# Kernel optimization log

Hardware: AMD Instinct MI355X
Metric: run time of the kernel (lower is better)

## Reference

```python
import jax, jax.numpy as jnp
import numpy as np
from jax import lax

EPS = 1e-5

def _conv(x, w, b, pad):
    # NCHW conv, stride 1, symmetric padding `pad`
    y = lax.conv_general_dilated(x, w, window_strides=(1, 1),
                                 padding=[(pad, pad), (pad, pad)],
                                 dimension_numbers=('NCHW', 'OIHW', 'NCHW'))
    return y + b[None, :, None, None]

def _bn(x, gamma, beta):
    # BatchNorm2d, training mode: batch statistics over (N,H,W)
    mean = jnp.mean(x, axis=(0, 2, 3), keepdims=True)
    var = jnp.var(x, axis=(0, 2, 3), keepdims=True)
    return gamma[None, :, None, None] * (x - mean) * lax.rsqrt(var + EPS) + beta[None, :, None, None]

def setup_inputs() -> dict:
    key = jax.random.key(0)
    ks = jax.random.split(key, 8)
    B, C, H, W = 4, 256, 64, 64
    OC = 256
    s3 = 1.0 / np.sqrt(C * 9)
    s1 = 1.0 / np.sqrt(C)
    return {
        'x': jax.random.normal(ks[0], (B, C, H, W), jnp.float32),
        'Wq': jax.random.normal(ks[1], (OC, C, 3, 3), jnp.float32) * s3,
        'bq': jnp.zeros((OC,), jnp.float32),
        'gq': jnp.ones((OC,), jnp.float32),
        'betaq': jnp.zeros((OC,), jnp.float32),
        'Wk': jax.random.normal(ks[2], (OC, C, 1, 1), jnp.float32) * s1,
        'bk': jnp.zeros((OC,), jnp.float32),
        'gk': jnp.ones((OC,), jnp.float32),
        'betak': jnp.zeros((OC,), jnp.float32),
        'Wv': jax.random.normal(ks[3], (OC, C, 1, 1), jnp.float32) * s1,
        'bv': jnp.zeros((OC,), jnp.float32),
        'gv': jnp.ones((OC,), jnp.float32),
        'betav': jnp.zeros((OC,), jnp.float32),
    }

def reference(x, Wq, bq, gq, betaq, Wk, bk, gk, betak, Wv, bv, gv, betav):
    # Q: 3x3 conv, pad 1 -> (b, oc, h, w); K,V: 1x1 conv with pad 1 -> (b, oc, h+2, w+2)
    Q = _bn(_conv(x, Wq, bq, 1), gq, betaq)
    K = _bn(_conv(x, Wk, bk, 1), gk, betak)
    V = _bn(_conv(x, Wv, bv, 1), gv, betav)
    b, oc, oh, ow = Q.shape
    q = Q.reshape(b, oc, oh * ow)          # (b, c, q_tokens)
    k = K.reshape(b, oc, -1)               # (b, c, k_tokens)
    v = V.reshape(b, oc, -1)               # (b, c, k_tokens)
    scores = jnp.einsum('bck,bcq->bkq', k, q)      # (b, k_tokens, q_tokens)
    attn = jax.nn.softmax(scores, axis=1)          # softmax over key tokens (dim=1)
    out = jnp.einsum('bck,bkq->bcq', v, attn)      # (b, c, q_tokens)
    return out.reshape(b, oc, oh, ow)
```

## Files before the change

kernel.cpp:

```cpp
#include <hip/hip_runtime.h>


typedef unsigned short u16;
typedef _Float16 f16x8 __attribute__((ext_vector_type(8)));
typedef __attribute__((ext_vector_type(4))) float f32x4;

__device__ __forceinline__ u16 f2h(float f) {
  _Float16 h = (_Float16)f;
  return *(const u16*)&h;
}
__device__ __forceinline__ float bf2f(u16 h) {
  return __uint_as_float(((unsigned)h) << 16);
}
__device__ __forceinline__ float ldin(const void* p, size_t i, int f32) {
  return f32 ? ((const float*)p)[i] : bf2f(((const u16*)p)[i]);
}
__device__ __forceinline__ u16 f2bf(float f) {
  unsigned u = __float_as_uint(f);
  u += 0x7fffu + ((u >> 16) & 1u);
  return (u16)(u >> 16);
}
__device__ __forceinline__ void gld16(const void* g, void* l) {
  __builtin_amdgcn_global_load_lds(
      (const __attribute__((address_space(1))) unsigned int*)g,
      (__attribute__((address_space(3))) unsigned int*)l, 16, 0, 0);
}

__global__ __launch_bounds__(256) void k_detect(const unsigned* __restrict__ w,
                                                int* __restrict__ flag) {
  __shared__ int red[4];
  int tid = threadIdx.x, cnt = 0;
#pragma unroll
  for (int j = 0; j < 8; j++) {
    unsigned e = (w[tid + j * 8192] >> 7) & 0xFFu;
    cnt += (e >= 118u && e <= 127u) ? 1 : 0;
  }
#pragma unroll
  for (int off = 32; off; off >>= 1) cnt += __shfl_down(cnt, off);
  if ((tid & 63) == 0) red[tid >> 6] = cnt;
  __syncthreads();
  if (tid == 0)
    flag[0] = (red[0] + red[1] + red[2] + red[3] < 625) ? 1 : 0;
}

__global__ __launch_bounds__(256) void k_txp(const void* __restrict__ x,
                                             const int* __restrict__ flag,
                                             u16* __restrict__ xbTp) {
  __shared__ float tile[32][33];
  int f32 = flag[0];
  int b = blockIdx.z, p0 = blockIdx.x * 32, c0 = blockIdx.y * 32;
  int tx = threadIdx.x, ty = threadIdx.y;
#pragma unroll
  for (int i = 0; i < 4; i++) {
    int c = c0 + ty + i * 8, pp = p0 + tx;
    float v = 0.f;
    if (pp < 4356) {
      int yy = pp / 66, xx = pp - yy * 66;
      if (yy >= 1 && yy <= 64 && xx >= 1 && xx <= 64)
        v = ldin(x, ((size_t)b * 256 + c) * 4096 + (yy - 1) * 64 + (xx - 1), f32);
    }
    tile[ty + i * 8][tx] = v;
  }
  __syncthreads();
#pragma unroll
  for (int i = 0; i < 4; i++) {
    int pp = p0 + ty + i * 8;
    if (pp >= 4356) continue;
    xbTp[((size_t)b * 4356 + pp) * 256 + c0 + tx] = f2h(tile[tx][ty + i * 8]);
  }
}

__global__ __launch_bounds__(256) void k_wq(const void* __restrict__ Wq,
                                            const int* __restrict__ flag,
                                            u16* __restrict__ WqB) {
  int idx = blockIdx.x * 256 + threadIdx.x;
  int oc = idx / 2304, rem = idx - oc * 2304;
  int tap = rem >> 8, c = rem & 255;
  WqB[idx] = f2h(ldin(Wq, oc * 2304 + c * 9 + tap, flag[0]));
}
__global__ __launch_bounds__(256) void k_wkv(const void* __restrict__ Wk,
                                             const void* __restrict__ Wv,
                                             const int* __restrict__ flag,
                                             u16* __restrict__ WkvB) {
  int idx = blockIdx.x * 256 + threadIdx.x;
  int m = idx >> 8, c = idx & 255;
  float w = (m < 256) ? ldin(Wk, m * 256 + c, flag[0])
                      : ldin(Wv, (m - 256) * 256 + c, flag[0]);
  WkvB[idx] = f2h(w);
}

template <bool IMC, int EPI, int SWZ>
__global__ __launch_bounds__(256, 3) void gemm_bt(
    const u16* __restrict__ A, const u16* __restrict__ Bt, void* __restrict__ Cptr,
    int M, int N, int K, int ldB, int tapBase, long long cOff, int kChunk,
    int sw1, int sw2, int nSplit, long long zA, long long zB, long long zC) {
  __shared__ u16 lA[128 * 64];
  __shared__ u16 lB[128 * 64];
  int tm, tn, b = 0, kz = 0;
  if (SWZ == 1) {
    int lin = blockIdx.x, xcd = lin & 7, per = lin >> 3;
    tm = xcd * sw1 + (per % sw1);
    tn = per / sw1;
    b = blockIdx.y;
  } else if (SWZ == 2) {
    int lin = blockIdx.x, xcd = lin & 7, per = lin >> 3;
    tm = per % sw1;
    tn = xcd * sw2 + per / sw1;
    kz = blockIdx.z;
  } else {
    tm = blockIdx.x;
    tn = blockIdx.y;
    b = blockIdx.z / nSplit;
    kz = blockIdx.z % nSplit;
  }
  int k0 = 0, k1 = K;
  if (kChunk) {
    k0 = kz * kChunk;
    k1 = min(k0 + kChunk, K);
  }
  const int tid = threadIdx.x, wave = tid >> 6, lane = tid & 63;
  const int sr = lane >> 3;
  const int scw = (lane & 7) ^ sr;
  const int wm = (wave >> 1) * 64, wn = (wave & 1) * 64;
  const int r16 = lane & 15, q = lane >> 4;
  const u16* gA = A + (size_t)b * zA + (size_t)(tm * 128 + wave * 32 + sr) * K +
                  scw * 8;
  const u16* gB = nullptr;
  int pyI[4], pxI[4];
  size_t bOffI[4];
  if (IMC) {
#pragma unroll
    for (int i = 0; i < 4; i++) {
      int n = tn * 128 + wave * 32 + i * 8 + sr;
      int bb = n >> 12, pix = n & 4095;
      pyI[i] = pix >> 6;
      pxI[i] = pix & 63;
      bOffI[i] = (size_t)bb * 4356;
    }
  } else {
    gB = Bt + (size_t)b * zB + (size_t)(tn * 128 + wave * 32 + sr) * ldB +
         scw * 8;
  }
  f32x4 acc[4][4] = {};

  for (int kt = k0; kt < k1; kt += 64) {
    int dy = 0, dx = 0, chunk = 0;
    if (IMC) {
      int tap = tapBase + (kt >> 8);
      chunk = kt & 255;
      dy = tap / 3;
      dx = tap - dy * 3;
    }
#pragma unroll
    for (int i = 0; i < 4; i++) {
      gld16(gA + (size_t)(i * 8) * K + kt, &lA[(wave * 32 + i * 8) * 64]);
      if (IMC) {
        int spix = (pyI[i] + dy) * 66 + pxI[i] + dx;
        gld16(Bt + (bOffI[i] + spix) * 256 + chunk + scw * 8,
              &lB[(wave * 32 + i * 8) * 64]);
      } else {
        gld16(gB + (size_t)(i * 8) * ldB + kt, &lB[(wave * 32 + i * 8) * 64]);
      }
    }
    __syncthreads();
#pragma unroll
    for (int ks = 0; ks < 64; ks += 32) {
      f16x8 af[4], bfr[4];
#pragma unroll
      for (int f = 0; f < 4; f++) {
        int ma = wm + f * 16 + r16;
        int g = (ks >> 3) + q;
        af[f] = *(const f16x8*)&lA[ma * 64 + ((g ^ (ma & 7)) << 3)];
        int nb = wn + f * 16 + r16;
        bfr[f] = *(const f16x8*)&lB[nb * 64 + ((g ^ (nb & 7)) << 3)];
      }
#pragma unroll
      for (int fi = 0; fi < 4; fi++)
#pragma unroll
        for (int fj = 0; fj < 4; fj++)
          acc[fi][fj] = __builtin_amdgcn_mfma_f32_16x16x32_f16(
              af[fi], bfr[fj], acc[fi][fj], 0, 0, 0);
    }
    __syncthreads();
  }

  const int colB = tn * 128 + wn + r16;
  const int rowB = tm * 128 + wm + q * 4;
  float* C = (float*)Cptr + cOff + (size_t)b * zC;
  if (EPI == 0) {
#pragma unroll
    for (int fi = 0; fi < 4; fi++)
#pragma unroll
      for (int r = 0; r < 4; r++) {
        size_t ro = (size_t)(rowB + fi * 16 + r) * N;
#pragma unroll
        for (int fj = 0; fj < 4; fj++) C[ro + colB + fj * 16] = acc[fi][fj][r];
      }
  } else {
#pragma unroll
    for (int fi = 0; fi < 4; fi++)
#pragma unroll
      for (int r = 0; r < 4; r++) {
        size_t ro = (size_t)(rowB + fi * 16 + r) * N;
#pragma unroll
        for (int fj = 0; fj < 4; fj++)
          atomicAdd(&C[ro + colB + fj * 16], acc[fi][fj][r]);
      }
  }
}

__global__ __launch_bounds__(256) void k_stats(
    const float* __restrict__ bufQ, const float* __restrict__ bufKV,
    const void* __restrict__ gq, const void* __restrict__ betaq,
    const void* __restrict__ gk, const void* __restrict__ betak,
    const void* __restrict__ gv, const void* __restrict__ betav,
    const int* __restrict__ flag, float* __restrict__ nrm) {
  int f32 = flag[0];
  int ch = blockIdx.x, t = blockIdx.y, tid = threadIdx.x;
  const float* row = (t == 0) ? bufQ + (size_t)ch * 16384
                              : bufKV + (size_t)(t == 1 ? ch : 256 + ch) * 16384;
  float s = 0.f, ss = 0.f;
  for (int i = tid; i < 16384; i += 256) {
    float v = row[i];
    s += v;
    ss += v * v;
  }
#pragma unroll
  for (int off = 32; off; off >>= 1) {
    s += __shfl_down(s, off);
    ss += __shfl_down(ss, off);
  }
  __shared__ float ls[4], lss[4];
  if ((tid & 63) == 0) {
    ls[tid >> 6] = s;
    lss[tid >> 6] = ss;
  }
  __syncthreads();
  if (tid == 0) {
    s = ls[0] + ls[1] + ls[2] + ls[3];
    ss = lss[0] + lss[1] + lss[2] + lss[3];
    float cnt = (t == 0) ? 16384.f : 17424.f;
    float mean = s / cnt;
    float var = fmaxf(ss / cnt - mean * mean, 0.f);
    const void* g = (t == 0) ? gq : (t == 1 ? gk : gv);
    const void* be = (t == 0) ? betaq : (t == 1 ? betak : betav);
    float sc = ldin(g, ch, f32) * rsqrtf(var + 1e-5f);
    nrm[(t * 256 + ch) * 2] = sc;
    nrm[(t * 256 + ch) * 2 + 1] = ldin(be, ch, f32) - mean * sc;
  }
}

__global__ __launch_bounds__(256) void k_qTs(const float* __restrict__ bufQ,
                                             const float* __restrict__ nrm,
                                             u16* __restrict__ qTs) {
  __shared__ u16 th[32][33];
  int b = blockIdx.z, q0 = blockIdx.x * 32, c0 = blockIdx.y * 32;
  int tx = threadIdx.x, ty = threadIdx.y;
#pragma unroll
  for (int i = 0; i < 4; i++) {
    int c = c0 + ty + i * 8;
    float sc = nrm[c * 2], sh = nrm[c * 2 + 1];
    th[ty + i * 8][tx] =
        f2h(bufQ[(size_t)c * 16384 + b * 4096 + q0 + tx] * sc + sh);
  }
  __syncthreads();
#pragma unroll
  for (int i = 0; i < 4; i++)
    qTs[((size_t)b * 4096 + q0 + ty + i * 8) * 256 + c0 + tx] =
        th[tx][ty + i * 8];
}
__global__ __launch_bounds__(256) void k_kTs(const float* __restrict__ bufKV,
                                             const float* __restrict__ nrm,
                                             u16* __restrict__ kTs) {
  __shared__ u16 th[32][33];
  int b = blockIdx.z, k0 = blockIdx.x * 32, c0 = blockIdx.y * 32;
  int tx = threadIdx.x, ty = threadIdx.y;
#pragma unroll
  for (int i = 0; i < 4; i++) {
    int c = c0 + ty + i * 8;
    int kt = k0 + tx;
    float v = 0.f;
    if (kt < 4356) {
      float sc = nrm[(256 + c) * 2], sh = nrm[(256 + c) * 2 + 1];
      int yy = kt / 66, xx = kt - yy * 66;
      if (yy >= 1 && yy <= 64 && xx >= 1 && xx <= 64)
        v = bufKV[(size_t)c * 16384 + b * 4096 + (yy - 1) * 64 + (xx - 1)] * sc + sh;
      else
        v = sh;
    }
    th[ty + i * 8][tx] = f2h(v);
  }
  __syncthreads();
#pragma unroll
  for (int i = 0; i < 4; i++)
    kTs[((size_t)b * 4480 + k0 + ty + i * 8) * 256 + c0 + tx] =
        th[tx][ty + i * 8];
}

__global__ __launch_bounds__(256) void k_vP(const float* __restrict__ bufKV,
                                            const float* __restrict__ nrm,
                                            u16* __restrict__ vP) {
  int b = blockIdx.z, ch = blockIdx.y;
  int kt = blockIdx.x * 256 + threadIdx.x;
  if (kt >= 4480) return;
  float v = 0.f;
  if (kt < 4356) {
    float sc = nrm[(512 + ch) * 2], sh = nrm[(512 + ch) * 2 + 1];
    int yy = kt / 66, xx = kt - yy * 66;
    if (yy >= 1 && yy <= 64 && xx >= 1 && xx <= 64)
      v = bufKV[(size_t)(256 + ch) * 16384 + b * 4096 + (yy - 1) * 64 + (xx - 1)] * sc + sh;
    else
      v = sh;
  }
  vP[((size_t)b * 256 + ch) * 4480 + kt] = f2h(v);
}

__global__ __launch_bounds__(256, 2) void k_flash(
    const u16* __restrict__ qTs, const u16* __restrict__ kTs,
    const u16* __restrict__ vP, float* __restrict__ Op,
    float* __restrict__ ml) {
  __shared__ u16 lS[2][16384];
  __shared__ u16 lP[64 * 128];
  const int lin = blockIdx.x;
  const int xcd = lin & 7, per = lin >> 3;
  const int h = xcd & 1, b = xcd >> 1;
  const int qt0 = per * 64;
  const int tid = threadIdx.x, wave = tid >> 6, lane = tid & 63;
  const int sr = lane >> 3, scw = (lane & 7) ^ sr;
  const int r16 = lane & 15, q = lane >> 4;

  const u16* gQ = qTs + ((size_t)b * 4096 + qt0 + wave * 16 + r16) * 256;
  f16x8 aq[8];
#pragma unroll
  for (int kk = 0; kk < 8; kk++) aq[kk] = *(const f16x8*)&gQ[kk * 32 + q * 8];
  asm volatile("s_waitcnt vmcnt(0)" ::: "memory");

  const u16* gK = kTs + (size_t)b * 4480 * 256 + (size_t)(wave * 32 + sr) * 256 + scw * 8;
  const u16* gV = vP + ((size_t)b * 256 + wave * 64 + sr) * 4480 + scw * 8;

#define STAGE_K(buf, kt, c2)                                                 \
  {                                                                          \
    _Pragma("unroll") for (int i = 0; i < 4; i++) {                          \
      const u16* src = gK + (size_t)((kt) + i * 8) * 256 + (c2) * 128;       \
      gld16(src, &lS[buf][(wave * 32 + i * 8) * 64]);                        \
      gld16(src + 64, &lS[buf][8192 + (wave * 32 + i * 8) * 64]);            \
    }                                                                        \
  }
#define STAGE_V(buf, kt, vc)                                                 \
  {                                                                          \
    _Pragma("unroll") for (int i = 0; i < 8; i++)                            \
        gld16(gV + (size_t)(i * 8) * 4480 + (kt) + (vc) * 64,                \
              &lS[buf][(wave * 64 + i * 8) * 64]);                           \
  }
#define WAITB(n)                                                             \
  asm volatile("s_waitcnt vmcnt(" #n ")" ::: "memory");                      \
  __builtin_amdgcn_s_barrier();                                              \
  __builtin_amdgcn_sched_barrier(0);
#define CLOSEB()                                                             \
  __builtin_amdgcn_sched_barrier(0);                                         \
  asm volatile("s_waitcnt lgkmcnt(0)" ::: "memory");                         \
  __builtin_amdgcn_s_barrier();

  f32x4 acc_o[16];
#pragma unroll
  for (int i = 0; i < 16; i++) acc_o[i] = (f32x4){0.f, 0.f, 0.f, 0.f};
  f32x4 m_v = {-3e38f, -3e38f, -3e38f, -3e38f};
  f32x4 l_v = {0.f, 0.f, 0.f, 0.f};

  const int ktBeg = h ? 2304 : 0, ktEnd = h ? 4480 : 2304;
  STAGE_K(0, ktBeg, 0);
  for (int kt0 = ktBeg; kt0 < ktEnd; kt0 += 128) {
    f32x4 acc_s[8];
#pragma unroll
    for (int i = 0; i < 8; i++) acc_s[i] = (f32x4){0.f, 0.f, 0.f, 0.f};
    STAGE_K(1, kt0, 1);
    WAITB(8);
    __builtin_amdgcn_s_setprio(1);
#pragma unroll
    for (int kcL = 0; kcL < 2; kcL++)
#pragma unroll
      for (int ks = 0; ks < 64; ks += 32)
#pragma unroll
        for (int fj = 0; fj < 8; fj++) {
          int nb = fj * 16 + r16;
          int g = (ks >> 3) + q;
          f16x8 bf = *(const f16x8*)&lS[0][kcL * 8192 + nb * 64 + ((g ^ (nb & 7)) << 3)];
          acc_s[fj] = __builtin_amdgcn_mfma_f32_16x16x32_f16(
              aq[kcL * 2 + (ks >> 5)], bf, acc_s[fj], 0, 0, 0);
        }
    __builtin_amdgcn_s_setprio(0);
    CLOSEB();
    STAGE_V(0, kt0, 0);
    WAITB(8);
    __builtin_amdgcn_s_setprio(1);
#pragma unroll
    for (int kcL = 0; kcL < 2; kcL++)
#pragma unroll
      for (int ks = 0; ks < 64; ks += 32)
#pragma unroll
        for (int fj = 0; fj < 8; fj++) {
          int nb = fj * 16 + r16;
          int g = (ks >> 3) + q;
          f16x8 bf = *(const f16x8*)&lS[1][kcL * 8192 + nb * 64 + ((g ^ (nb & 7)) << 3)];
          acc_s[fj] = __builtin_amdgcn_mfma_f32_16x16x32_f16(
              aq[4 + kcL * 2 + (ks >> 5)], bf, acc_s[fj], 0, 0, 0);
        }
    __builtin_amdgcn_s_setprio(0);
    CLOSEB();
    STAGE_V(1, kt0, 1);
    if (kt0 + 128 > 4356) {
#pragma unroll
      for (int fj = 0; fj < 8; fj++)
        if (kt0 + fj * 16 + r16 >= 4356)
          acc_s[fj] = (f32x4){-1e30f, -1e30f, -1e30f, -1e30f};
    }
    f32x4 pm = acc_s[0];
#pragma unroll
    for (int fj = 1; fj < 8; fj++)
#pragma unroll
      for (int rr = 0; rr < 4; rr++) pm[rr] = fmaxf(pm[rr], acc_s[fj][rr]);
#pragma unroll
    for (int d = 1; d < 16; d <<= 1)
#pragma unroll
      for (int rr = 0; rr < 4; rr++)
        pm[rr] = fmaxf(pm[rr], __shfl_xor(pm[rr], d));
    int need = !__all(pm[0] - m_v[0] <= 8.f && pm[1] - m_v[1] <= 8.f &&
                      pm[2] - m_v[2] <= 8.f && pm[3] - m_v[3] <= 8.f);
    if (need) {
      f32x4 fac;
#pragma unroll
      for (int rr = 0; rr < 4; rr++) {
        float mn = fmaxf(m_v[rr], pm[rr]);
        fac[rr] = __expf(m_v[rr] - mn);
        m_v[rr] = mn;
        l_v[rr] *= fac[rr];
      }
#pragma unroll
      for (int fj = 0; fj < 16; fj++)
#pragma unroll
        for (int rr = 0; rr < 4; rr++) acc_o[fj][rr] *= fac[rr];
    }
    f32x4 rs = {0.f, 0.f, 0.f, 0.f};
#pragma unroll
    for (int fj = 0; fj < 8; fj++)
#pragma unroll
      for (int rr = 0; rr < 4; rr++) {
        _Float16 hp = (_Float16)__expf(acc_s[fj][rr] - m_v[rr]);
        rs[rr] += (float)hp;
        int row = wave * 16 + q * 4 + rr;
        int c8 = fj * 2 + (r16 >> 3);
        lP[row * 128 + (((c8 ^ (row & 15)) << 3) | (r16 & 7))] = *(const u16*)&hp;
      }
#pragma unroll
    for (int d = 1; d < 16; d <<= 1)
#pragma unroll
      for (int rr = 0; rr < 4; rr++) rs[rr] += __shfl_xor(rs[rr], d);
#pragma unroll
    for (int rr = 0; rr < 4; rr++) l_v[rr] += rs[rr];
    WAITB(8);
    __builtin_amdgcn_s_setprio(1);
#pragma unroll
    for (int ks = 0; ks < 64; ks += 32) {
      int k8 = (ks >> 3) + q;
      f16x8 ap = *(const f16x8*)&lP[(wave * 16 + r16) * 128 + ((k8 ^ r16) << 3)];
#pragma unroll
      for (int fj = 0; fj < 16; fj++) {
        int nb = fj * 16 + r16;
        int g = (ks >> 3) + q;
        f16x8 bv = *(const f16x8*)&lS[0][nb * 64 + ((g ^ (nb & 7)) << 3)];
        acc_o[fj] = __builtin_amdgcn_mfma_f32_16x16x32_f16(ap, bv, acc_o[fj], 0, 0, 0);
      }
    }
    __builtin_amdgcn_s_setprio(0);
    CLOSEB();
    if (kt0 + 128 < ktEnd) {
      STAGE_K(0, kt0 + 128, 0);
      WAITB(8);
    } else {
      WAITB(0);
    }
    __builtin_amdgcn_s_setprio(1);
#pragma unroll
    for (int ks = 0; ks < 64; ks += 32) {
      int k8 = 8 + (ks >> 3) + q;
      f16x8 ap = *(const f16x8*)&lP[(wave * 16 + r16) * 128 + ((k8 ^ r16) << 3)];
#pragma unroll
      for (int fj = 0; fj < 16; fj++) {
        int nb = fj * 16 + r16;
        int g = (ks >> 3) + q;
        f16x8 bv = *(const f16x8*)&lS[1][nb * 64 + ((g ^ (nb & 7)) << 3)];
        acc_o[fj] = __builtin_amdgcn_mfma_f32_16x16x32_f16(ap, bv, acc_o[fj], 0, 0, 0);
      }
    }
    __builtin_amdgcn_s_setprio(0);
    CLOSEB();
  }
#undef STAGE_K
#undef STAGE_V
#undef WAITB
#undef CLOSEB
  size_t ob = ((size_t)(h * 4 + b) * 4096 + qt0 + wave * 16) * 256;
#pragma unroll
  for (int rr = 0; rr < 4; rr++) {
    size_t rowo = ob + (size_t)(q * 4 + rr) * 256;
#pragma unroll
    for (int fj = 0; fj < 16; fj++) Op[rowo + fj * 16 + r16] = acc_o[fj][rr];
  }
  if (r16 == 0) {
    int base = (h * 4 + b) * 4096 + qt0 + wave * 16 + q * 4;
    *(f32x4*)&ml[base] = m_v;
    *(f32x4*)&ml[32768 + base] = l_v;
  }
}

__global__ __launch_bounds__(256) void k_merge(const float* __restrict__ Op,
                                               const float* __restrict__ ml,
                                               const int* __restrict__ flag,
                                               void* __restrict__ out) {
  __shared__ float th[32][33];
  int b = blockIdx.z, qt0 = blockIdx.x * 32, c0 = blockIdx.y * 32;
  int tx = threadIdx.x, ty = threadIdx.y;
#pragma unroll
  for (int i = 0; i < 4; i++) {
    int qt = qt0 + ty + i * 8;
    float m0 = ml[b * 4096 + qt], m1 = ml[(4 + b) * 4096 + qt];
    float l0 = ml[32768 + b * 4096 + qt], l1 = ml[32768 + (4 + b) * 4096 + qt];
    float M = fmaxf(m0, m1);
    float e0 = __expf(m0 - M), e1 = __expf(m1 - M);
    float inv = 1.f / (l0 * e0 + l1 * e1);
    float v = (Op[((size_t)b * 4096 + qt) * 256 + c0 + tx] * e0 +
               Op[((size_t)(4 + b) * 4096 + qt) * 256 + c0 + tx] * e1) * inv;
    v = (v == v) ? v : 0.f;
    th[ty + i * 8][tx] = v;
  }
  __syncthreads();
#pragma unroll
  for (int i = 0; i < 4; i++) {
    int c = c0 + ty + i * 8, qt = qt0 + tx;
    float v = th[tx][ty + i * 8];
    size_t oidx = ((size_t)b * 256 + c) * 4096 + qt;
    if (flag[0])
      ((float*)out)[oidx] = v;
    else
      ((u16*)out)[oidx] = f2bf(v);
  }
}

__global__ __launch_bounds__(256) void k_zeroacc(float* __restrict__ accF) {
  accF[blockIdx.x * 256 + threadIdx.x] = 0.f;
}

extern "C" void kernel_launch(void* const* d_in, const int* in_sizes, int n_in,
                              void* d_out, int out_size, void* d_ws, size_t ws_size,
                              hipStream_t stream) {
  const void* x = d_in[0];
  const void* Wq = d_in[1];
  const void* gq = d_in[3];
  const void* betaq = d_in[4];
  const void* Wk = d_in[5];
  const void* gk = d_in[7];
  const void* betak = d_in[8];
  const void* Wv = d_in[9];
  const void* gv = d_in[11];
  const void* betav = d_in[12];

  char* ws = (char*)d_ws;
  int* flag = (int*)ws;
  u16* xbTp = (u16*)(ws + 256);
  u16* WqB = (u16*)(ws + 8921344);
  u16* WkvB = (u16*)(ws + 10100992);
  float* bufQ = (float*)(ws + 10363136);
  float* bufKV = (float*)(ws + 27140352);
  u16* qTs = (u16*)(ws + 60694784);
  u16* kTs = (u16*)(ws + 69083392);
  u16* vP = (u16*)(ws + 78258432);
  float* nrm = (float*)(ws + 87433472);
  float* Opart = (float*)(ws + 256);
  float* mlbuf = (float*)(ws + 33554688);

  dim3 b32x8(32, 8);
  k_detect<<<1, 256, 0, stream>>>((const unsigned*)Wq, flag);
  k_txp<<<dim3(137, 8, 4), b32x8, 0, stream>>>(x, flag, xbTp);
  k_wq<<<2304, 256, 0, stream>>>(Wq, flag, WqB);
  k_wkv<<<512, 256, 0, stream>>>(Wk, Wv, flag, WkvB);
  k_zeroacc<<<16384, 256, 0, stream>>>(bufQ);
  gemm_bt<true, 1, 2><<<dim3(256, 1, 3), 256, 0, stream>>>(
      WqB, xbTp, bufQ, 256, 16384, 2304, 0, 0, 0, 768, 2, 16, 1, 0, 0, 0);
  gemm_bt<true, 0, 2><<<512, 256, 0, stream>>>(
      WkvB, xbTp, bufKV, 512, 16384, 256, 0, 4, 0, 0, 4, 16, 1, 0, 0, 0);
  k_stats<<<dim3(256, 3), 256, 0, stream>>>(bufQ, bufKV, gq, betaq, gk, betak,
                                            gv, betav, flag, nrm);
  k_qTs<<<dim3(128, 8, 4), b32x8, 0, stream>>>(bufQ, nrm, qTs);
  k_kTs<<<dim3(140, 8, 4), b32x8, 0, stream>>>(bufKV, nrm, kTs);
  k_vP<<<dim3(18, 256, 4), 256, 0, stream>>>(bufKV, nrm, vP);
  k_flash<<<512, 256, 0, stream>>>(qTs, kTs, vP, Opart, mlbuf);
  k_merge<<<dim3(128, 8, 4), b32x8, 0, stream>>>(Opart, mlbuf, flag, d_out);
}
```

Before: 340.3 us.

## Double flash-attention query tile per block to reuse staged K/V tiles

Each flash block now processes 128 query tokens (32 per wave, two 16-row fragments) instead of 64, so every K and V tile staged into LDS feeds twice as many MFMAs. This halves global/LDS traffic for K and V per unit of work. In exchange, register pressure doubles (accumulators, Q fragments), occupancy drops to one block per CU, and the grid shrinks to 256 blocks, which on a 256-CU part leaves one wave group per CU with less latency hiding.

```diff
diff --git a/kernel.cpp b/kernel.cpp
--- a/kernel.cpp
+++ b/kernel.cpp
@@ -315,24 +315,27 @@
   vP[((size_t)b * 256 + ch) * 4480 + kt] = f2h(v);
 }
 
-__global__ __launch_bounds__(256, 2) void k_flash(
+__global__ __launch_bounds__(256, 1) void k_flash(
     const u16* __restrict__ qTs, const u16* __restrict__ kTs,
     const u16* __restrict__ vP, float* __restrict__ Op,
     float* __restrict__ ml) {
   __shared__ u16 lS[2][16384];
-  __shared__ u16 lP[64 * 128];
+  __shared__ u16 lP[128 * 128];
   const int lin = blockIdx.x;
   const int xcd = lin & 7, per = lin >> 3;
   const int h = xcd & 1, b = xcd >> 1;
-  const int qt0 = per * 64;
+  const int qt0 = per * 128;
   const int tid = threadIdx.x, wave = tid >> 6, lane = tid & 63;
   const int sr = lane >> 3, scw = (lane & 7) ^ sr;
   const int r16 = lane & 15, q = lane >> 4;
 
-  const u16* gQ = qTs + ((size_t)b * 4096 + qt0 + wave * 16 + r16) * 256;
-  f16x8 aq[8];
-#pragma unroll
-  for (int kk = 0; kk < 8; kk++) aq[kk] = *(const f16x8*)&gQ[kk * 32 + q * 8];
+  const u16* gQ = qTs + ((size_t)b * 4096 + qt0 + wave * 32 + r16) * 256;
+  f16x8 aq[2][8];
+#pragma unroll
+  for (int fi = 0; fi < 2; fi++)
+#pragma unroll
+    for (int kk = 0; kk < 8; kk++)
+      aq[fi][kk] = *(const f16x8*)&gQ[fi * 16 * 256 + kk * 32 + q * 8];
   asm volatile("s_waitcnt vmcnt(0)" ::: "memory");
 
   const u16* gK = kTs + (size_t)b * 4480 * 256 + (size_t)(wave * 32 + sr) * 256 + scw * 8;
@@ -361,18 +364,26 @@
   asm volatile("s_waitcnt lgkmcnt(0)" ::: "memory");                         \
   __builtin_amdgcn_s_barrier();
 
-  f32x4 acc_o[16];
-#pragma unroll
-  for (int i = 0; i < 16; i++) acc_o[i] = (f32x4){0.f, 0.f, 0.f, 0.f};
-  f32x4 m_v = {-3e38f, -3e38f, -3e38f, -3e38f};
-  f32x4 l_v = {0.f, 0.f, 0.f, 0.f};
+  f32x4 acc_o[2][16];
+#pragma unroll
+  for (int fi = 0; fi < 2; fi++)
+#pragma unroll
+    for (int i = 0; i < 16; i++) acc_o[fi][i] = (f32x4){0.f, 0.f, 0.f, 0.f};
+  f32x4 m_v[2], l_v[2];
+#pragma unroll
+  for (int fi = 0; fi < 2; fi++) {
+    m_v[fi] = (f32x4){-3e38f, -3e38f, -3e38f, -3e38f};
+    l_v[fi] = (f32x4){0.f, 0.f, 0.f, 0.f};
+  }
 
   const int ktBeg = h ? 2304 : 0, ktEnd = h ? 4480 : 2304;
   STAGE_K(0, ktBeg, 0);
   for (int kt0 = ktBeg; kt0 < ktEnd; kt0 += 128) {
-    f32x4 acc_s[8];
-#pragma unroll
-    for (int i = 0; i < 8; i++) acc_s[i] = (f32x4){0.f, 0.f, 0.f, 0.f};
+    f32x4 acc_s[2][8];
+#pragma unroll
+    for (int fi = 0; fi < 2; fi++)
+#pragma unroll
+      for (int i = 0; i < 8; i++) acc_s[fi][i] = (f32x4){0.f, 0.f, 0.f, 0.f};
     STAGE_K(1, kt0, 1);
     WAITB(8);
     __builtin_amdgcn_s_setprio(1);
@@ -385,8 +396,10 @@
           int nb = fj * 16 + r16;
           int g = (ks >> 3) + q;
           f16x8 bf = *(const f16x8*)&lS[0][kcL * 8192 + nb * 64 + ((g ^ (nb & 7)) << 3)];
-          acc_s[fj] = __builtin_amdgcn_mfma_f32_16x16x32_f16(
-              aq[kcL * 2 + (ks >> 5)], bf, acc_s[fj], 0, 0, 0);
+#pragma unroll
+          for (int fi = 0; fi < 2; fi++)
+            acc_s[fi][fj] = __builtin_amdgcn_mfma_f32_16x16x32_f16(
+                aq[fi][kcL * 2 + (ks >> 5)], bf, acc_s[fi][fj], 0, 0, 0);
         }
     __builtin_amdgcn_s_setprio(0);
     CLOSEB();
@@ -402,8 +415,10 @@
           int nb = fj * 16 + r16;
           int g = (ks >> 3) + q;
           f16x8 bf = *(const f16x8*)&lS[1][kcL * 8192 + nb * 64 + ((g ^ (nb & 7)) << 3)];
-          acc_s[fj] = __builtin_amdgcn_mfma_f32_16x16x32_f16(
-              aq[4 + kcL * 2 + (ks >> 5)], bf, acc_s[fj], 0, 0, 0);
+#pragma unroll
+          for (int fi = 0; fi < 2; fi++)
+            acc_s[fi][fj] = __builtin_amdgcn_mfma_f32_16x16x32_f16(
+                aq[fi][4 + kcL * 2 + (ks >> 5)], bf, acc_s[fi][fj], 0, 0, 0);
         }
     __builtin_amdgcn_s_setprio(0);
     CLOSEB();
@@ -412,63 +427,81 @@
 #pragma unroll
       for (int fj = 0; fj < 8; fj++)
         if (kt0 + fj * 16 + r16 >= 4356)
-          acc_s[fj] = (f32x4){-1e30f, -1e30f, -1e30f, -1e30f};
-    }
-    f32x4 pm = acc_s[0];
-#pragma unroll
-    for (int fj = 1; fj < 8; fj++)
-#pragma unroll
-      for (int rr = 0; rr < 4; rr++) pm[rr] = fmaxf(pm[rr], acc_s[fj][rr]);
-#pragma unroll
-    for (int d = 1; d < 16; d <<= 1)
-#pragma unroll
-      for (int rr = 0; rr < 4; rr++)
-        pm[rr] = fmaxf(pm[rr], __shfl_xor(pm[rr], d));
-    int need = !__all(pm[0] - m_v[0] <= 8.f && pm[1] - m_v[1] <= 8.f &&
-                      pm[2] - m_v[2] <= 8.f && pm[3] - m_v[3] <= 8.f);
+#pragma unroll
+          for (int fi = 0; fi < 2; fi++)
+            acc_s[fi][fj] = (f32x4){-1e30f, -1e30f, -1e30f, -1e30f};
+    }
+    f32x4 pm[2];
+#pragma unroll
+    for (int fi = 0; fi < 2; fi++) {
+      pm[fi] = acc_s[fi][0];
+#pragma unroll
+      for (int fj = 1; fj < 8; fj++)
+#pragma unroll
+        for (int rr = 0; rr < 4; rr++)
+          pm[fi][rr] = fmaxf(pm[fi][rr], acc_s[fi][fj][rr]);
+#pragma unroll
+      for (int d = 1; d < 16; d <<= 1)
+#pragma unroll
+        for (int rr = 0; rr < 4; rr++)
+          pm[fi][rr] = fmaxf(pm[fi][rr], __shfl_xor(pm[fi][rr], d));
+    }
+    int need = !__all(
+        pm[0][0] - m_v[0][0] <= 8.f && pm[0][1] - m_v[0][1] <= 8.f &&
+        pm[0][2] - m_v[0][2] <= 8.f && pm[0][3] - m_v[0][3] <= 8.f &&
+        pm[1][0] - m_v[1][0] <= 8.f && pm[1][1] - m_v[1][1] <= 8.f &&
+        pm[1][2] - m_v[1][2] <= 8.f && pm[1][3] - m_v[1][3] <= 8.f);
     if (need) {
-      f32x4 fac;
-#pragma unroll
-      for (int rr = 0; rr < 4; rr++) {
-        float mn = fmaxf(m_v[rr], pm[rr]);
-        fac[rr] = __expf(m_v[rr] - mn);
-        m_v[rr] = mn;
-        l_v[rr] *= fac[rr];
+#pragma unroll
+      for (int fi = 0; fi < 2; fi++) {
+        f32x4 fac;
+#pragma unroll
+        for (int rr = 0; rr < 4; rr++) {
+          float mn = fmaxf(m_v[fi][rr], pm[fi][rr]);
+          fac[rr] = __expf(m_v[fi][rr] - mn);
+          m_v[fi][rr] = mn;
+          l_v[fi][rr] *= fac[rr];
+        }
+#pragma unroll
+        for (int fj = 0; fj < 16; fj++)
+#pragma unroll
+          for (int rr = 0; rr < 4; rr++) acc_o[fi][fj][rr] *= fac[rr];
       }
-#pragma unroll
-      for (int fj = 0; fj < 16; fj++)
-#pragma unroll
-        for (int rr = 0; rr < 4; rr++) acc_o[fj][rr] *= fac[rr];
-    }
-    f32x4 rs = {0.f, 0.f, 0.f, 0.f};
-#pragma unroll
-    for (int fj = 0; fj < 8; fj++)
-#pragma unroll
-      for (int rr = 0; rr < 4; rr++) {
-        _Float16 hp = (_Float16)__expf(acc_s[fj][rr] - m_v[rr]);
-        rs[rr] += (float)hp;
-        int row = wave * 16 + q * 4 + rr;
-        int c8 = fj * 2 + (r16 >> 3);
-        lP[row * 128 + (((c8 ^ (row & 15)) << 3) | (r16 & 7))] = *(const u16*)&hp;
-      }
-#pragma unroll
-    for (int d = 1; d < 16; d <<= 1)
-#pragma unroll
-      for (int rr = 0; rr < 4; rr++) rs[rr] += __shfl_xor(rs[rr], d);
-#pragma unroll
-    for (int rr = 0; rr < 4; rr++) l_v[rr] += rs[rr];
+    }
+#pragma unroll
+    for (int fi = 0; fi < 2; fi++) {
+      f32x4 rs = {0.f, 0.f, 0.f, 0.f};
+#pragma unroll
+      for (int fj = 0; fj < 8; fj++)
+#pragma unroll
+        for (int rr = 0; rr < 4; rr++) {
+          _Float16 hp = (_Float16)__expf(acc_s[fi][fj][rr] - m_v[fi][rr]);
+          rs[rr] += (float)hp;
+          int row = wave * 32 + fi * 16 + q * 4 + rr;
+          int c8 = fj * 2 + (r16 >> 3);
+          lP[row * 128 + (((c8 ^ (row & 15)) << 3) | (r16 & 7))] = *(const u16*)&hp;
+        }
+#pragma unroll
+      for (int d = 1; d < 16; d <<= 1)
+#pragma unroll
+        for (int rr = 0; rr < 4; rr++) rs[rr] += __shfl_xor(rs[rr], d);
+#pragma unroll
+      for (int rr = 0; rr < 4; rr++) l_v[fi][rr] += rs[rr];
+    }
     WAITB(8);
     __builtin_amdgcn_s_setprio(1);
 #pragma unroll
     for (int ks = 0; ks < 64; ks += 32) {
       int k8 = (ks >> 3) + q;
-      f16x8 ap = *(const f16x8*)&lP[(wave * 16 + r16) * 128 + ((k8 ^ r16) << 3)];
+      f16x8 ap0 = *(const f16x8*)&lP[(wave * 32 + r16) * 128 + ((k8 ^ r16) << 3)];
+      f16x8 ap1 = *(const f16x8*)&lP[(wave * 32 + 16 + r16) * 128 + ((k8 ^ r16) << 3)];
 #pragma unroll
       for (int fj = 0; fj < 16; fj++) {
         int nb = fj * 16 + r16;
         int g = (ks >> 3) + q;
         f16x8 bv = *(const f16x8*)&lS[0][nb * 64 + ((g ^ (nb & 7)) << 3)];
-        acc_o[fj] = __builtin_amdgcn_mfma_f32_16x16x32_f16(ap, bv, acc_o[fj], 0, 0, 0);
+        acc_o[0][fj] = __builtin_amdgcn_mfma_f32_16x16x32_f16(ap0, bv, acc_o[0][fj], 0, 0, 0);
+        acc_o[1][fj] = __builtin_amdgcn_mfma_f32_16x16x32_f16(ap1, bv, acc_o[1][fj], 0, 0, 0);
       }
     }
     __builtin_amdgcn_s_setprio(0);
@@ -483,13 +516,15 @@
 #pragma unroll
     for (int ks = 0; ks < 64; ks += 32) {
       int k8 = 8 + (ks >> 3) + q;
-      f16x8 ap = *(const f16x8*)&lP[(wave * 16 + r16) * 128 + ((k8 ^ r16) << 3)];
+      f16x8 ap0 = *(const f16x8*)&lP[(wave * 32 + r16) * 128 + ((k8 ^ r16) << 3)];
+      f16x8 ap1 = *(const f16x8*)&lP[(wave * 32 + 16 + r16) * 128 + ((k8 ^ r16) << 3)];
 #pragma unroll
       for (int fj = 0; fj < 16; fj++) {
         int nb = fj * 16 + r16;
         int g = (ks >> 3) + q;
         f16x8 bv = *(const f16x8*)&lS[1][nb * 64 + ((g ^ (nb & 7)) << 3)];
-        acc_o[fj] = __builtin_amdgcn_mfma_f32_16x16x32_f16(ap, bv, acc_o[fj], 0, 0, 0);
+        acc_o[0][fj] = __builtin_amdgcn_mfma_f32_16x16x32_f16(ap0, bv, acc_o[0][fj], 0, 0, 0);
+        acc_o[1][fj] = __builtin_amdgcn_mfma_f32_16x16x32_f16(ap1, bv, acc_o[1][fj], 0, 0, 0);
       }
     }
     __builtin_amdgcn_s_setprio(0);
@@ -499,17 +534,20 @@
 #undef STAGE_V
 #undef WAITB
 #undef CLOSEB
-  size_t ob = ((size_t)(h * 4 + b) * 4096 + qt0 + wave * 16) * 256;
-#pragma unroll
-  for (int rr = 0; rr < 4; rr++) {
-    size_t rowo = ob + (size_t)(q * 4 + rr) * 256;
-#pragma unroll
-    for (int fj = 0; fj < 16; fj++) Op[rowo + fj * 16 + r16] = acc_o[fj][rr];
-  }
-  if (r16 == 0) {
-    int base = (h * 4 + b) * 4096 + qt0 + wave * 16 + q * 4;
-    *(f32x4*)&ml[base] = m_v;
-    *(f32x4*)&ml[32768 + base] = l_v;
+#pragma unroll
+  for (int fi = 0; fi < 2; fi++) {
+    size_t ob = ((size_t)(h * 4 + b) * 4096 + qt0 + wave * 32 + fi * 16) * 256;
+#pragma unroll
+    for (int rr = 0; rr < 4; rr++) {
+      size_t rowo = ob + (size_t)(q * 4 + rr) * 256;
+#pragma unroll
+      for (int fj = 0; fj < 16; fj++) Op[rowo + fj * 16 + r16] = acc_o[fi][fj][rr];
+    }
+    if (r16 == 0) {
+      int base = (h * 4 + b) * 4096 + qt0 + wave * 32 + fi * 16 + q * 4;
+      *(f32x4*)&ml[base] = m_v[fi];
+      *(f32x4*)&ml[32768 + base] = l_v[fi];
+    }
   }
 }
 
@@ -593,6 +631,6 @@
   k_qTs<<<dim3(128, 8, 4), b32x8, 0, stream>>>(bufQ, nrm, qTs);
   k_kTs<<<dim3(140, 8, 4), b32x8, 0, stream>>>(bufKV, nrm, kTs);
   k_vP<<<dim3(18, 256, 4), 256, 0, stream>>>(bufKV, nrm, vP);
-  k_flash<<<512, 256, 0, stream>>>(qTs, kTs, vP, Opart, mlbuf);
+  k_flash<<<256, 256, 0, stream>>>(qTs, kTs, vP, Opart, mlbuf);
   k_merge<<<dim3(128, 8, 4), b32x8, 0, stream>>>(Opart, mlbuf, flag, d_out);
 }
```

New measurement: 407.7 us. 19.8% more time.

## Double-buffer LDS in conv GEMMs and raise split-K for Q conv

Applied to the files above, without the earlier changes.

Adds a double-buffered LDS variant of the GEMM kernel that issues the global-to-LDS loads for the next K tile before computing the current one. Manual vmcnt waits and raw barriers replace the two __syncthreads per iteration. The Q 3x3 conv GEMM also moves from 3 to 4 K splits (kChunk 768 to 576), giving more blocks in exchange for more atomic accumulation. Doubling LDS to 64KB per block may lower occupancy below the 3 blocks per CU the launch bounds target.

```diff
diff --git a/kernel.cpp b/kernel.cpp
--- a/kernel.cpp
+++ b/kernel.cpp
@@ -89,13 +89,13 @@
   WkvB[idx] = f2h(w);
 }
 
-template <bool IMC, int EPI, int SWZ>
+template <bool IMC, int EPI, int SWZ, bool DB>
 __global__ __launch_bounds__(256, 3) void gemm_bt(
     const u16* __restrict__ A, const u16* __restrict__ Bt, void* __restrict__ Cptr,
     int M, int N, int K, int ldB, int tapBase, long long cOff, int kChunk,
     int sw1, int sw2, int nSplit, long long zA, long long zB, long long zC) {
-  __shared__ u16 lA[128 * 64];
-  __shared__ u16 lB[128 * 64];
+  __shared__ u16 lA[(DB ? 2 : 1) * 128 * 64];
+  __shared__ u16 lB[(DB ? 2 : 1) * 128 * 64];
   int tm, tn, b = 0, kz = 0;
   if (SWZ == 1) {
     int lin = blockIdx.x, xcd = lin & 7, per = lin >> 3;
@@ -143,7 +143,7 @@
   }
   f32x4 acc[4][4] = {};
 
-  for (int kt = k0; kt < k1; kt += 64) {
+  auto stage = [&](u16* dA, u16* dB, int kt) {
     int dy = 0, dx = 0, chunk = 0;
     if (IMC) {
       int tap = tapBase + (kt >> 8);
@@ -153,16 +153,17 @@
     }
 #pragma unroll
     for (int i = 0; i < 4; i++) {
-      gld16(gA + (size_t)(i * 8) * K + kt, &lA[(wave * 32 + i * 8) * 64]);
+      gld16(gA + (size_t)(i * 8) * K + kt, &dA[(wave * 32 + i * 8) * 64]);
       if (IMC) {
         int spix = (pyI[i] + dy) * 66 + pxI[i] + dx;
         gld16(Bt + (bOffI[i] + spix) * 256 + chunk + scw * 8,
-              &lB[(wave * 32 + i * 8) * 64]);
+              &dB[(wave * 32 + i * 8) * 64]);
       } else {
-        gld16(gB + (size_t)(i * 8) * ldB + kt, &lB[(wave * 32 + i * 8) * 64]);
-      }
-    }
-    __syncthreads();
+        gld16(gB + (size_t)(i * 8) * ldB + kt, &dB[(wave * 32 + i * 8) * 64]);
+      }
+    }
+  };
+  auto compute = [&](const u16* sA, const u16* sB) {
 #pragma unroll
     for (int ks = 0; ks < 64; ks += 32) {
       f16x8 af[4], bfr[4];
@@ -170,9 +171,9 @@
       for (int f = 0; f < 4; f++) {
         int ma = wm + f * 16 + r16;
         int g = (ks >> 3) + q;
-        af[f] = *(const f16x8*)&lA[ma * 64 + ((g ^ (ma & 7)) << 3)];
+        af[f] = *(const f16x8*)&sA[ma * 64 + ((g ^ (ma & 7)) << 3)];
         int nb = wn + f * 16 + r16;
-        bfr[f] = *(const f16x8*)&lB[nb * 64 + ((g ^ (nb & 7)) << 3)];
+        bfr[f] = *(const f16x8*)&sB[nb * 64 + ((g ^ (nb & 7)) << 3)];
       }
 #pragma unroll
       for (int fi = 0; fi < 4; fi++)
@@ -181,7 +182,33 @@
           acc[fi][fj] = __builtin_amdgcn_mfma_f32_16x16x32_f16(
               af[fi], bfr[fj], acc[fi][fj], 0, 0, 0);
     }
-    __syncthreads();
+  };
+
+  if (DB) {
+    stage(lA, lB, k0);
+    int cur = 0;
+    for (int kt = k0; kt < k1; kt += 64) {
+      if (kt + 64 < k1) {
+        stage(&lA[(cur ^ 1) * 8192], &lB[(cur ^ 1) * 8192], kt + 64);
+        asm volatile("s_waitcnt vmcnt(8)" ::: "memory");
+      } else {
+        asm volatile("s_waitcnt vmcnt(0)" ::: "memory");
+      }
+      __builtin_amdgcn_s_barrier();
+      __builtin_amdgcn_sched_barrier(0);
+      compute(&lA[cur * 8192], &lB[cur * 8192]);
+      __builtin_amdgcn_sched_barrier(0);
+      asm volatile("s_waitcnt lgkmcnt(0)" ::: "memory");
+      __builtin_amdgcn_s_barrier();
+      cur ^= 1;
+    }
+  } else {
+    for (int kt = k0; kt < k1; kt += 64) {
+      stage(lA, lB, kt);
+      __syncthreads();
+      compute(lA, lB);
+      __syncthreads();
+    }
   }
 
   const int colB = tn * 128 + wn + r16;
@@ -584,9 +611,9 @@
   k_wq<<<2304, 256, 0, stream>>>(Wq, flag, WqB);
   k_wkv<<<512, 256, 0, stream>>>(Wk, Wv, flag, WkvB);
   k_zeroacc<<<16384, 256, 0, stream>>>(bufQ);
-  gemm_bt<true, 1, 2><<<dim3(256, 1, 3), 256, 0, stream>>>(
-      WqB, xbTp, bufQ, 256, 16384, 2304, 0, 0, 0, 768, 2, 16, 1, 0, 0, 0);
-  gemm_bt<true, 0, 2><<<512, 256, 0, stream>>>(
+  gemm_bt<true, 1, 2, true><<<dim3(256, 1, 4), 256, 0, stream>>>(
+      WqB, xbTp, bufQ, 256, 16384, 2304, 0, 0, 0, 576, 2, 16, 1, 0, 0, 0);
+  gemm_bt<true, 0, 2, true><<<512, 256, 0, stream>>>(
       WkvB, xbTp, bufKV, 512, 16384, 256, 0, 4, 0, 0, 4, 16, 1, 0, 0, 0);
   k_stats<<<dim3(256, 3), 256, 0, stream>>>(bufQ, bufKV, gq, betaq, gk, betak,
                                             gv, betav, flag, nrm);
```

Result: slower. 349.3 us (+2.6%).

## Repartition PV matmul so each wave owns a channel slice across all query rows

Applied to the files above, without the earlier changes.

The P·V stage is re-tiled so each wave computes all 64 query rows for its own 64-channel slice, instead of 16 query rows across all 256 channels. Each V fragment loaded from LDS is now reused across four MFMAs rather than one. The rescale factors therefore have to be shared through a new LDS array, and the P tile is halved and written in two passes, with the second half kept in registers until after the first barrier. This cuts LDS read traffic for V, at the cost of extra barriers with lgkmcnt waits and unconditional rescaling of the accumulators every iteration.

```diff
diff --git a/kernel.cpp b/kernel.cpp
--- a/kernel.cpp
+++ b/kernel.cpp
@@ -320,7 +320,8 @@
     const u16* __restrict__ vP, float* __restrict__ Op,
     float* __restrict__ ml) {
   __shared__ u16 lS[2][16384];
-  __shared__ u16 lP[64 * 128];
+  __shared__ u16 lP[64 * 64];
+  __shared__ float lFac[64];
   const int lin = blockIdx.x;
   const int xcd = lin & 7, per = lin >> 3;
   const int h = xcd & 1, b = xcd >> 1;
@@ -353,7 +354,7 @@
               &lS[buf][(wave * 64 + i * 8) * 64]);                           \
   }
 #define WAITB(n)                                                             \
-  asm volatile("s_waitcnt vmcnt(" #n ")" ::: "memory");                      \
+  asm volatile("s_waitcnt vmcnt(" #n ") lgkmcnt(0)" ::: "memory");           \
   __builtin_amdgcn_s_barrier();                                              \
   __builtin_amdgcn_sched_barrier(0);
 #define CLOSEB()                                                             \
@@ -361,9 +362,11 @@
   asm volatile("s_waitcnt lgkmcnt(0)" ::: "memory");                         \
   __builtin_amdgcn_s_barrier();
 
-  f32x4 acc_o[16];
-#pragma unroll
-  for (int i = 0; i < 16; i++) acc_o[i] = (f32x4){0.f, 0.f, 0.f, 0.f};
+  f32x4 acc_o[4][4];
+#pragma unroll
+  for (int mt = 0; mt < 4; mt++)
+#pragma unroll
+    for (int fj = 0; fj < 4; fj++) acc_o[mt][fj] = (f32x4){0.f, 0.f, 0.f, 0.f};
   f32x4 m_v = {-3e38f, -3e38f, -3e38f, -3e38f};
   f32x4 l_v = {0.f, 0.f, 0.f, 0.f};
 
@@ -426,8 +429,8 @@
         pm[rr] = fmaxf(pm[rr], __shfl_xor(pm[rr], d));
     int need = !__all(pm[0] - m_v[0] <= 8.f && pm[1] - m_v[1] <= 8.f &&
                       pm[2] - m_v[2] <= 8.f && pm[3] - m_v[3] <= 8.f);
+    f32x4 fac = {1.f, 1.f, 1.f, 1.f};
     if (need) {
-      f32x4 fac;
 #pragma unroll
       for (int rr = 0; rr < 4; rr++) {
         float mn = fmaxf(m_v[rr], pm[rr]);
@@ -435,11 +438,9 @@
         m_v[rr] = mn;
         l_v[rr] *= fac[rr];
       }
-#pragma unroll
-      for (int fj = 0; fj < 16; fj++)
-#pragma unroll
-        for (int rr = 0; rr < 4; rr++) acc_o[fj][rr] *= fac[rr];
-    }
+    }
+    if (r16 == 0) *(f32x4*)&lFac[wave * 16 + q * 4] = fac;
+    _Float16 hq[4][4];
     f32x4 rs = {0.f, 0.f, 0.f, 0.f};
 #pragma unroll
     for (int fj = 0; fj < 8; fj++)
@@ -448,8 +449,12 @@
         _Float16 hp = (_Float16)__expf(acc_s[fj][rr] - m_v[rr]);
         rs[rr] += (float)hp;
         int row = wave * 16 + q * 4 + rr;
-        int c8 = fj * 2 + (r16 >> 3);
-        lP[row * 128 + (((c8 ^ (row & 15)) << 3) | (r16 & 7))] = *(const u16*)&hp;
+        if (fj < 4) {
+          int c8 = fj * 2 + (r16 >> 3);
+          lP[row * 64 + (((c8 ^ (row & 7)) << 3) | (r16 & 7))] = *(const u16*)&hp;
+        } else {
+          hq[fj - 4][rr] = hp;
+        }
       }
 #pragma unroll
     for (int d = 1; d < 16; d <<= 1)
@@ -458,21 +463,45 @@
 #pragma unroll
     for (int rr = 0; rr < 4; rr++) l_v[rr] += rs[rr];
     WAITB(8);
+    f32x4 facv[4];
+#pragma unroll
+    for (int mt = 0; mt < 4; mt++)
+      facv[mt] = *(const f32x4*)&lFac[mt * 16 + q * 4];
+#pragma unroll
+    for (int mt = 0; mt < 4; mt++)
+#pragma unroll
+      for (int fj = 0; fj < 4; fj++)
+#pragma unroll
+        for (int rr = 0; rr < 4; rr++) acc_o[mt][fj][rr] *= facv[mt][rr];
     __builtin_amdgcn_s_setprio(1);
 #pragma unroll
     for (int ks = 0; ks < 64; ks += 32) {
       int k8 = (ks >> 3) + q;
-      f16x8 ap = *(const f16x8*)&lP[(wave * 16 + r16) * 128 + ((k8 ^ r16) << 3)];
-#pragma unroll
-      for (int fj = 0; fj < 16; fj++) {
-        int nb = fj * 16 + r16;
-        int g = (ks >> 3) + q;
-        f16x8 bv = *(const f16x8*)&lS[0][nb * 64 + ((g ^ (nb & 7)) << 3)];
-        acc_o[fj] = __builtin_amdgcn_mfma_f32_16x16x32_f16(ap, bv, acc_o[fj], 0, 0, 0);
+      f16x8 ap[4];
+#pragma unroll
+      for (int mt = 0; mt < 4; mt++)
+        ap[mt] = *(const f16x8*)&lP[(mt * 16 + r16) * 64 + ((k8 ^ (r16 & 7)) << 3)];
+#pragma unroll
+      for (int fj = 0; fj < 4; fj++) {
+        int cr = wave * 64 + fj * 16 + r16;
+        f16x8 bv = *(const f16x8*)&lS[0][cr * 64 + ((k8 ^ (cr & 7)) << 3)];
+#pragma unroll
+        for (int mt = 0; mt < 4; mt++)
+          acc_o[mt][fj] = __builtin_amdgcn_mfma_f32_16x16x32_f16(
+              ap[mt], bv, acc_o[mt][fj], 0, 0, 0);
       }
     }
     __builtin_amdgcn_s_setprio(0);
     CLOSEB();
+#pragma unroll
+    for (int fj = 0; fj < 4; fj++)
+#pragma unroll
+      for (int rr = 0; rr < 4; rr++) {
+        int row = wave * 16 + q * 4 + rr;
+        int c8 = fj * 2 + (r16 >> 3);
+        lP[row * 64 + (((c8 ^ (row & 7)) << 3) | (r16 & 7))] =
+            *(const u16*)&hq[fj][rr];
+      }
     if (kt0 + 128 < ktEnd) {
       STAGE_K(0, kt0 + 128, 0);
       WAITB(8);
@@ -482,14 +511,19 @@
     __builtin_amdgcn_s_setprio(1);
 #pragma unroll
     for (int ks = 0; ks < 64; ks += 32) {
-      int k8 = 8 + (ks >> 3) + q;
-      f16x8 ap = *(const f16x8*)&lP[(wave * 16 + r16) * 128 + ((k8 ^ r16) << 3)];
-#pragma unroll
-      for (int fj = 0; fj < 16; fj++) {
-        int nb = fj * 16 + r16;
-        int g = (ks >> 3) + q;
-        f16x8 bv = *(const f16x8*)&lS[1][nb * 64 + ((g ^ (nb & 7)) << 3)];
-        acc_o[fj] = __builtin_amdgcn_mfma_f32_16x16x32_f16(ap, bv, acc_o[fj], 0, 0, 0);
+      int k8 = (ks >> 3) + q;
+      f16x8 ap[4];
+#pragma unroll
+      for (int mt = 0; mt < 4; mt++)
+        ap[mt] = *(const f16x8*)&lP[(mt * 16 + r16) * 64 + ((k8 ^ (r16 & 7)) << 3)];
+#pragma unroll
+      for (int fj = 0; fj < 4; fj++) {
+        int cr = wave * 64 + fj * 16 + r16;
+        f16x8 bv = *(const f16x8*)&lS[1][cr * 64 + ((k8 ^ (cr & 7)) << 3)];
+#pragma unroll
+        for (int mt = 0; mt < 4; mt++)
+          acc_o[mt][fj] = __builtin_amdgcn_mfma_f32_16x16x32_f16(
+              ap[mt], bv, acc_o[mt][fj], 0, 0, 0);
       }
     }
     __builtin_amdgcn_s_setprio(0);
@@ -499,13 +533,16 @@
 #undef STAGE_V
 #undef WAITB
 #undef CLOSEB
-  size_t ob = ((size_t)(h * 4 + b) * 4096 + qt0 + wave * 16) * 256;
-#pragma unroll
-  for (int rr = 0; rr < 4; rr++) {
-    size_t rowo = ob + (size_t)(q * 4 + rr) * 256;
-#pragma unroll
-    for (int fj = 0; fj < 16; fj++) Op[rowo + fj * 16 + r16] = acc_o[fj][rr];
-  }
+  size_t obase = ((size_t)(h * 4 + b) * 4096 + qt0) * 256;
+#pragma unroll
+  for (int mt = 0; mt < 4; mt++)
+#pragma unroll
+    for (int rr = 0; rr < 4; rr++) {
+      size_t rowo = obase + (size_t)(mt * 16 + q * 4 + rr) * 256;
+#pragma unroll
+      for (int fj = 0; fj < 4; fj++)
+        Op[rowo + wave * 64 + fj * 16 + r16] = acc_o[mt][fj][rr];
+    }
   if (r16 == 0) {
     int base = (h * 4 + b) * 4096 + qt0 + wave * 16 + q * 4;
     *(f32x4*)&ml[base] = m_v;
```

After: 347.7 us. +2.2%, slower.
